# Kernel optimization log

Measured on AMD Instinct MI355X. Metric: run time of the kernel, lower is better.

The kernel has to match this reference:

```python
import jax, jax.numpy as jnp
import numpy as np

B, S, E, H = 2, 2048, 1024, 16
DK = E // H


def setup_inputs() -> dict:
    key = jax.random.key(0)
    ks = jax.random.split(key, 12)
    scale = 1.0 / np.sqrt(E)
    return {
        "query": jax.random.normal(ks[0], (B, S, E), jnp.float32),
        "key": jax.random.normal(ks[1], (B, S, E), jnp.float32),
        "value": jax.random.normal(ks[2], (B, S, E), jnp.float32),
        "key_padding_mask": jnp.ones((B, S, S), jnp.int32),
        "Wq": jax.random.normal(ks[3], (E, E), jnp.float32) * scale,
        "bq": jax.random.normal(ks[4], (E,), jnp.float32) * scale,
        "Wk": jax.random.normal(ks[5], (E, E), jnp.float32) * scale,
        "bk": jax.random.normal(ks[6], (E,), jnp.float32) * scale,
        "Wv": jax.random.normal(ks[7], (E, E), jnp.float32) * scale,
        "bv": jax.random.normal(ks[8], (E,), jnp.float32) * scale,
        "Wo": jax.random.normal(ks[9], (E, E), jnp.float32) * scale,
        "bo": jax.random.normal(ks[10], (E,), jnp.float32) * scale,
    }


def reference(query, key, value, key_padding_mask, Wq, bq, Wk, bk, Wv, bv, Wo, bo):
    b = query.shape[0]
    # torch Linear: x @ W.T + b ; then split heads -> [b, h, t, d_k]
    q = (query @ Wq.T + bq).reshape(b, -1, H, DK).transpose(0, 2, 1, 3)
    k = (key @ Wk.T + bk).reshape(b, -1, H, DK).transpose(0, 2, 1, 3)
    v = (value @ Wv.T + bv).reshape(b, -1, H, DK).transpose(0, 2, 1, 3)
    scores = jnp.einsum("bhqd,bhkd->bhqk", q, k) / np.sqrt(DK)  # [b,h,Tq,Tk]
    mask = (key_padding_mask[:, None, :, :] == 0)  # [b,1,Tq,Tk]
    scores = jnp.where(mask, -jnp.inf, scores)
    attn = jax.nn.softmax(scores, axis=-1)
    attn = jnp.where(mask, 0.0, attn)
    x = jnp.einsum("bhqk,bhkd->bhqd", attn, v)  # [b,h,Tq,d_k]
    x = x.transpose(0, 2, 1, 3).reshape(b, -1, H * DK)  # [b,Tq,E]
    return x @ Wo.T + bo
```

## Files before the change

### kernel.cpp

```cpp
#include <hip/hip_runtime.h>
#include <hip/hip_bf16.h>
#include <cstdint>
#include <cstddef>

#define BB 2
#define SS 2048
#define EE 1024
#define HH 16
#define DKK 64

typedef __bf16 bf16;
typedef __bf16 bf16x8 __attribute__((ext_vector_type(8)));
typedef float f32x4 __attribute__((ext_vector_type(4)));

__device__ __forceinline__ void ldg2lds16(const void* g, void* l) {
  __builtin_amdgcn_global_load_lds(
      (const __attribute__((address_space(1))) unsigned int*)g,
      (__attribute__((address_space(3))) unsigned int*)l, 16, 0, 0);
}

__global__ __launch_bounds__(256) void detect_kernel(
    const unsigned int* __restrict__ q, int* __restrict__ flag) {
  const int t = threadIdx.x;
  int cnt = 0;
#pragma unroll
  for (int i = 0; i < 4; i++) {
    unsigned int v = q[t * 4 + i];
    unsigned int e = (v >> 7) & 0xFF;
    cnt += (e >= 110 && e <= 140) ? 1 : 0;
  }
  __shared__ int s;
  if (t == 0) s = 0;
  __syncthreads();
  atomicAdd(&s, cnt);
  __syncthreads();
  if (t == 0) *flag = (s < 512) ? 1 : 0;
}

struct ConvArgs {
  const void* src[11];
  void* dst[11];
  int n[11];
};

__global__ __launch_bounds__(256) void convert_kernel(
    ConvArgs a, const int* __restrict__ flag) {
  const int j = blockIdx.y;
  const int n = a.n[j];
  const int i0 = (blockIdx.x * 256 + threadIdx.x) * 8;
  if (i0 >= n) return;
  bf16* d = (bf16*)a.dst[j];
  if (*flag) {
    const float* s = (const float*)a.src[j];
    float4 f0 = ((const float4*)(s + i0))[0];
    float4 f1 = ((const float4*)(s + i0))[1];
    union { bf16 h[8]; uint4 u; } t;
    t.h[0] = (bf16)f0.x; t.h[1] = (bf16)f0.y;
    t.h[2] = (bf16)f0.z; t.h[3] = (bf16)f0.w;
    t.h[4] = (bf16)f1.x; t.h[5] = (bf16)f1.y;
    t.h[6] = (bf16)f1.z; t.h[7] = (bf16)f1.w;
    *(uint4*)(d + i0) = t.u;
  } else {
    uint4 v = *(const uint4*)((const bf16*)a.src[j] + i0);
    *(uint4*)(d + i0) = v;
  }
}

__global__ __launch_bounds__(256) void mask_summary_kernel(
    const int* __restrict__ mask, unsigned char* __restrict__ msum) {
  const int bid = blockIdx.x;
  const int kt = bid & 31;
  const int qt = (bid >> 5) & 15;
  const int b = bid >> 9;
  const int t = threadIdx.x;
  const int r = t >> 1;
  const int c0 = (t & 1) * 32;
  const int* p = mask + ((size_t)(b * SS + qt * 128 + r)) * SS + kt * 64 + c0;
  bool all1 = true, any1 = false;
#pragma unroll
  for (int i = 0; i < 8; i++) {
    int4 v = ((const int4*)p)[i];
    all1 = all1 && (v.x != 0) && (v.y != 0) && (v.z != 0) && (v.w != 0);
    any1 = any1 || (v.x != 0) || (v.y != 0) || (v.z != 0) || (v.w != 0);
  }
  __shared__ int sall, sany;
  if (t == 0) { sall = 1; sany = 0; }
  __syncthreads();
  if (!all1) atomicAnd(&sall, 0);
  if (any1) atomicOr(&sany, 1);
  __syncthreads();
  if (t == 0) msum[bid] = sall ? 1 : (sany ? 2 : 0);
}

template <int BM, int BN, int WGM, int WGN, typename OutT>
__device__ __forceinline__ void gemm_bt_core(
    const bf16* __restrict__ A, const bf16* __restrict__ W,
    const bf16* __restrict__ bias, OutT* __restrict__ out, int mode) {
  constexpr int BK = 32;
  constexpr int WM = BM / WGM, WN = BN / WGN;
  constexpr int MI = WM / 16, NI = WN / 16;
  constexpr int Kd = 1024, Nd = 1024;

  __shared__ __align__(16) bf16 As[BM * BK];
  __shared__ __align__(16) bf16 Bs[BN * BK];

  const int tid = threadIdx.x;
  const int wid = tid >> 6, lane = tid & 63;
  const int lr = lane & 15, lg = lane >> 4;
  const int wm = (wid / WGN) * WM, wn = (wid % WGN) * WN;
  const int m0 = blockIdx.y * BM, n0 = blockIdx.x * BN;

  f32x4 acc[MI][NI] = {};

  const int sr = tid >> 2;
  const int scol = (tid & 3) * 8;

  for (int k0 = 0; k0 < Kd; k0 += BK) {
#pragma unroll
    for (int i = 0; i < BM / 64; i++)
      ldg2lds16(A + (size_t)(m0 + sr + i * 64) * Kd + k0 + scol,
                &As[(sr + i * 64) * BK + scol]);
#pragma unroll
    for (int i = 0; i < BN / 64; i++)
      ldg2lds16(W + (size_t)(n0 + sr + i * 64) * Kd + k0 + scol,
                &Bs[(sr + i * 64) * BK + scol]);
    __syncthreads();
    bf16x8 af[MI], bfr[NI];
#pragma unroll
    for (int mi = 0; mi < MI; mi++)
      af[mi] = *(const bf16x8*)&As[(wm + mi * 16 + lr) * BK + lg * 8];
#pragma unroll
    for (int ni = 0; ni < NI; ni++)
      bfr[ni] = *(const bf16x8*)&Bs[(wn + ni * 16 + lr) * BK + lg * 8];
#pragma unroll
    for (int mi = 0; mi < MI; mi++)
#pragma unroll
      for (int ni = 0; ni < NI; ni++)
        acc[mi][ni] = __builtin_amdgcn_mfma_f32_16x16x32_bf16(
            af[mi], bfr[ni], acc[mi][ni], 0, 0, 0);
    __syncthreads();
  }

  const float scale = (mode == 1) ? 0.125f : 1.0f;

#pragma unroll
  for (int ni = 0; ni < NI; ni++) {
    const int n = n0 + wn + ni * 16 + lr;
    const float bv = (float)bias[n];
#pragma unroll
    for (int mi = 0; mi < MI; mi++) {
      const int m = m0 + wm + mi * 16 + lg * 4;
      f32x4 v = acc[mi][ni];
      if (mode == 2) {
        const int h = n >> 6, d = n & 63;
        const int b = m >> 11, s0v = m & 2047;
        union { bf16 hh[4]; uint2 u; } tmp;
#pragma unroll
        for (int r = 0; r < 4; r++) tmp.hh[r] = (bf16)(v[r] + bv);
        const size_t idx = (((size_t)b * HH + h) * DKK + d) * SS + s0v;
        *(uint2*)((bf16*)out + idx) = tmp.u;
      } else {
#pragma unroll
        for (int r = 0; r < 4; r++)
          out[(size_t)(m + r) * Nd + n] = (OutT)((v[r] + bv) * scale);
      }
    }
  }
}

__global__ __launch_bounds__(256) void qkv_proj_kernel(
    const bf16* __restrict__ q, const bf16* __restrict__ k,
    const bf16* __restrict__ v, const bf16* __restrict__ Wq,
    const bf16* __restrict__ Wk, const bf16* __restrict__ Wv,
    const bf16* __restrict__ bias4, bf16* __restrict__ Qo,
    bf16* __restrict__ Ko, bf16* __restrict__ Vto) {
  const int z = blockIdx.z;
  const bf16* A = z == 0 ? q : (z == 1 ? k : v);
  const bf16* W = z == 0 ? Wq : (z == 1 ? Wk : Wv);
  const bf16* bi = bias4 + z * 1024;
  bf16* out = z == 0 ? Qo : (z == 1 ? Ko : Vto);
  gemm_bt_core<128, 128, 2, 2, bf16>(A, W, bi, out, z == 0 ? 1 : (z == 1 ? 0 : 2));
}

__global__ __launch_bounds__(256) void o_proj_kernel(
    const bf16* __restrict__ X, const bf16* __restrict__ Wo,
    const bf16* __restrict__ bo, float* __restrict__ out) {
  gemm_bt_core<64, 128, 1, 4, float>(X, Wo, bo, out, 0);
}

__global__ __launch_bounds__(256, 4) void flash_kernel(
    const bf16* __restrict__ Qb, const bf16* __restrict__ Kb,
    const bf16* __restrict__ Vt, const int* __restrict__ mask,
    const unsigned char* __restrict__ msum, bf16* __restrict__ X) {
  const int flat = blockIdx.x;
  const int bh = flat & 31;
  const int qt2 = flat >> 5;
  const int b = bh >> 4;
  const int h = bh & 15;

  const bf16* Qg = Qb + ((size_t)(b * SS + qt2 * 64)) * EE + h * 64;
  const bf16* Kg = Kb + ((size_t)(b * SS)) * EE + h * 64;
  const bf16* Vg = Vt + ((size_t)(b * HH + h)) * DKK * SS;

  __shared__ __align__(16) bf16 QPs[4608];
  __shared__ __align__(16) bf16 Ks[2 * 64 * 32];
  __shared__ __align__(16) bf16 Vs[2 * 64 * 32];

  const int tid = threadIdx.x;
  const int wid = tid >> 6, lane = tid & 63;
  const int lr = lane & 15, lg = lane >> 4;

#pragma unroll
  for (int j = 0; j < 2; j++) {
    const int u = j * 256 + tid;
    const int kk = u >> 8, row = (u >> 2) & 63, c = (u & 3) * 8;
    ldg2lds16(Qg + (size_t)row * EE + kk * 32 + c, &QPs[u * 8]);
  }
  __syncthreads();

  bf16x8 qf[2];
#pragma unroll
  for (int kk = 0; kk < 2; kk++)
    qf[kk] = *(const bf16x8*)&QPs[kk * 2048 + (wid * 16 + lr) * 32 + lg * 8];
  __syncthreads();

  float mrow[4], lrow[4];
  f32x4 ot[4] = {};
#pragma unroll
  for (int r = 0; r < 4; r++) { mrow[r] = -1e30f; lrow[r] = 0.f; }

  bf16* Pw = &QPs[wid * 1152];

  for (int kt = 0; kt < SS / 64; kt++) {
    const unsigned char sm = msum[(b * 16 + (qt2 >> 1)) * 32 + kt];
    if (sm == 0) continue;

#pragma unroll
    for (int j = 0; j < 2; j++) {
      const int u = j * 256 + tid;
      const int kk = u >> 8, row = (u >> 2) & 63, c = (u & 3) * 8;
      ldg2lds16(Kg + (size_t)(kt * 64 + row) * EE + kk * 32 + c, &Ks[u * 8]);
      ldg2lds16(Vg + (size_t)row * SS + kt * 64 + kk * 32 + c, &Vs[u * 8]);
    }
    __syncthreads();

    f32x4 sc[4] = {};
#pragma unroll
    for (int kk = 0; kk < 2; kk++)
#pragma unroll
      for (int ni = 0; ni < 4; ni++) {
        const bf16x8 kf =
            *(const bf16x8*)&Ks[kk * 2048 + (ni * 16 + lr) * 32 + lg * 8];
        sc[ni] = __builtin_amdgcn_mfma_f32_16x16x32_bf16(qf[kk], kf, sc[ni],
                                                         0, 0, 0);
      }

    if (sm == 2) {
#pragma unroll
      for (int ni = 0; ni < 4; ni++)
#pragma unroll
        for (int r = 0; r < 4; r++) {
          const int qq = qt2 * 64 + wid * 16 + lg * 4 + r;
          const int kk2 = kt * 64 + ni * 16 + lr;
          if (mask[((size_t)b * SS + qq) * SS + kk2] == 0) sc[ni][r] = -1e30f;
        }
    }

    float al[4], mn[4], rs[4];
#pragma unroll
    for (int r = 0; r < 4; r++) {
      float t = fmaxf(fmaxf(sc[0][r], sc[1][r]), fmaxf(sc[2][r], sc[3][r]));
#pragma unroll
      for (int off = 8; off >= 1; off >>= 1) t = fmaxf(t, __shfl_xor(t, off));
      mn[r] = fmaxf(mrow[r], t);
      al[r] = __expf(mrow[r] - mn[r]);
      mrow[r] = mn[r];
      rs[r] = 0.f;
    }
    if (sm == 2) {
#pragma unroll
      for (int ni = 0; ni < 4; ni++)
#pragma unroll
        for (int r = 0; r < 4; r++) {
          const float pv =
              (sc[ni][r] > -5e29f) ? __expf(sc[ni][r] - mn[r]) : 0.f;
          rs[r] += pv;
          Pw[(lg * 4 + r) * 72 + ni * 16 + lr] = (bf16)pv;
        }
    } else {
#pragma unroll
      for (int ni = 0; ni < 4; ni++)
#pragma unroll
        for (int r = 0; r < 4; r++) {
          const float pv = __expf(sc[ni][r] - mn[r]);
          rs[r] += pv;
          Pw[(lg * 4 + r) * 72 + ni * 16 + lr] = (bf16)pv;
        }
    }
#pragma unroll
    for (int r = 0; r < 4; r++) {
#pragma unroll
      for (int off = 8; off >= 1; off >>= 1) rs[r] += __shfl_xor(rs[r], off);
      lrow[r] = lrow[r] * al[r] + rs[r];
    }

#pragma unroll
    for (int di = 0; di < 4; di++)
#pragma unroll
      for (int r = 0; r < 4; r++) ot[di][r] *= al[r];

#pragma unroll
    for (int kk = 0; kk < 2; kk++) {
      const bf16x8 pf = *(const bf16x8*)&Pw[lr * 72 + kk * 32 + lg * 8];
#pragma unroll
      for (int di = 0; di < 4; di++) {
        const bf16x8 vf =
            *(const bf16x8*)&Vs[kk * 2048 + (di * 16 + lr) * 32 + lg * 8];
        ot[di] = __builtin_amdgcn_mfma_f32_16x16x32_bf16(pf, vf, ot[di],
                                                         0, 0, 0);
      }
    }
    __syncthreads();
  }

#pragma unroll
  for (int r = 0; r < 4; r++) {
    const float linv = (lrow[r] > 0.f) ? 1.0f / lrow[r] : 0.f;
    const int q = qt2 * 64 + wid * 16 + lg * 4 + r;
    bf16* xp = X + ((size_t)b * SS + q) * EE + h * 64;
#pragma unroll
    for (int di = 0; di < 4; di++)
      xp[di * 16 + lr] = (bf16)(ot[di][r] * linv);
  }
}

extern "C" void kernel_launch(void* const* d_in, const int* in_sizes, int n_in,
                              void* d_out, int out_size, void* d_ws,
                              size_t ws_size, hipStream_t stream) {
  const int* mask = (const int*)d_in[3];

  const size_t NIN = (size_t)BB * SS * EE;
  const size_t NW = (size_t)EE * EE;

  char* p = (char*)d_ws;
  bf16* cq = (bf16*)p;   p += NIN * 2;
  bf16* ck = (bf16*)p;   p += NIN * 2;
  bf16* cv = (bf16*)p;   p += NIN * 2;
  bf16* cWq = (bf16*)p;  p += NW * 2;
  bf16* cWk = (bf16*)p;  p += NW * 2;
  bf16* cWv = (bf16*)p;  p += NW * 2;
  bf16* cWo = (bf16*)p;  p += NW * 2;
  bf16* cb = (bf16*)p;   p += 4 * 1024 * 2;
  unsigned char* msum = (unsigned char*)p; p += 1024;
  int* flag = (int*)p;   p += 1024;
  bf16* Qb = (bf16*)p;   p += NIN * 2;
  bf16* Kb = (bf16*)p;   p += NIN * 2;
  bf16* Vt = (bf16*)p;   p += NIN * 2;
  bf16* X = (bf16*)p;    p += NIN * 2;

  const size_t need = (size_t)(p - (char*)d_ws);
  if (ws_size < need) return;

  detect_kernel<<<dim3(1), dim3(256), 0, stream>>>(
      (const unsigned int*)d_in[0], flag);

  ConvArgs ca;
  ca.src[0] = d_in[0];   ca.dst[0] = cq;        ca.n[0] = (int)NIN;
  ca.src[1] = d_in[1];   ca.dst[1] = ck;        ca.n[1] = (int)NIN;
  ca.src[2] = d_in[2];   ca.dst[2] = cv;        ca.n[2] = (int)NIN;
  ca.src[3] = d_in[4];   ca.dst[3] = cWq;       ca.n[3] = (int)NW;
  ca.src[4] = d_in[6];   ca.dst[4] = cWk;       ca.n[4] = (int)NW;
  ca.src[5] = d_in[8];   ca.dst[5] = cWv;       ca.n[5] = (int)NW;
  ca.src[6] = d_in[10];  ca.dst[6] = cWo;       ca.n[6] = (int)NW;
  ca.src[7] = d_in[5];   ca.dst[7] = cb;        ca.n[7] = 1024;
  ca.src[8] = d_in[7];   ca.dst[8] = cb + 1024; ca.n[8] = 1024;
  ca.src[9] = d_in[9];   ca.dst[9] = cb + 2048; ca.n[9] = 1024;
  ca.src[10] = d_in[11]; ca.dst[10] = cb + 3072; ca.n[10] = 1024;
  convert_kernel<<<dim3(2048, 11), dim3(256), 0, stream>>>(ca, flag);

  mask_summary_kernel<<<dim3(BB * 16 * 32), dim3(256), 0, stream>>>(mask, msum);

  qkv_proj_kernel<<<dim3(8, 32, 3), dim3(256), 0, stream>>>(
      cq, ck, cv, cWq, cWk, cWv, cb, Qb, Kb, Vt);

  flash_kernel<<<dim3(1024), dim3(256), 0, stream>>>(
      Qb, Kb, Vt, mask, msum, X);

  o_proj_kernel<<<dim3(8, 64), dim3(256), 0, stream>>>(X, cWo, cb + 3072,
                                                       (float*)d_out);
}
```

Measured before the change: 322.4 us.

## Enlarge flash query tile to 128 rows and XOR-swizzle LDS chunks

```diff
diff --git a/kernel.cpp b/kernel.cpp
--- a/kernel.cpp
+++ b/kernel.cpp
@@ -113,25 +113,26 @@
   f32x4 acc[MI][NI] = {};
 
   const int sr = tid >> 2;
-  const int scol = (tid & 3) * 8;
+  const int scol = ((tid & 3) ^ (sr & 3)) * 8;
+  const int rchunk = (lg ^ (lr & 3)) * 8;
 
   for (int k0 = 0; k0 < Kd; k0 += BK) {
 #pragma unroll
     for (int i = 0; i < BM / 64; i++)
       ldg2lds16(A + (size_t)(m0 + sr + i * 64) * Kd + k0 + scol,
-                &As[(sr + i * 64) * BK + scol]);
+                &As[(sr + i * 64) * BK + (tid & 3) * 8]);
 #pragma unroll
     for (int i = 0; i < BN / 64; i++)
       ldg2lds16(W + (size_t)(n0 + sr + i * 64) * Kd + k0 + scol,
-                &Bs[(sr + i * 64) * BK + scol]);
+                &Bs[(sr + i * 64) * BK + (tid & 3) * 8]);
     __syncthreads();
     bf16x8 af[MI], bfr[NI];
 #pragma unroll
     for (int mi = 0; mi < MI; mi++)
-      af[mi] = *(const bf16x8*)&As[(wm + mi * 16 + lr) * BK + lg * 8];
+      af[mi] = *(const bf16x8*)&As[(wm + mi * 16 + lr) * BK + rchunk];
 #pragma unroll
     for (int ni = 0; ni < NI; ni++)
-      bfr[ni] = *(const bf16x8*)&Bs[(wn + ni * 16 + lr) * BK + lg * 8];
+      bfr[ni] = *(const bf16x8*)&Bs[(wn + ni * 16 + lr) * BK + rchunk];
 #pragma unroll
     for (int mi = 0; mi < MI; mi++)
 #pragma unroll
@@ -188,149 +189,178 @@
   gemm_bt_core<64, 128, 1, 4, float>(X, Wo, bo, out, 0);
 }
 
-__global__ __launch_bounds__(256, 4) void flash_kernel(
+__global__ __launch_bounds__(256, 2) void flash_kernel(
     const bf16* __restrict__ Qb, const bf16* __restrict__ Kb,
     const bf16* __restrict__ Vt, const int* __restrict__ mask,
     const unsigned char* __restrict__ msum, bf16* __restrict__ X) {
   const int flat = blockIdx.x;
   const int bh = flat & 31;
-  const int qt2 = flat >> 5;
+  const int qt = flat >> 5;
   const int b = bh >> 4;
   const int h = bh & 15;
 
-  const bf16* Qg = Qb + ((size_t)(b * SS + qt2 * 64)) * EE + h * 64;
+  const bf16* Qg = Qb + ((size_t)(b * SS + qt * 128)) * EE + h * 64;
   const bf16* Kg = Kb + ((size_t)(b * SS)) * EE + h * 64;
   const bf16* Vg = Vt + ((size_t)(b * HH + h)) * DKK * SS;
 
-  __shared__ __align__(16) bf16 QPs[4608];
-  __shared__ __align__(16) bf16 Ks[2 * 64 * 32];
-  __shared__ __align__(16) bf16 Vs[2 * 64 * 32];
+  __shared__ __align__(16) bf16 QPs[8704];
+  __shared__ __align__(16) bf16 Ks[4096];
+  __shared__ __align__(16) bf16 Vs[4096];
 
   const int tid = threadIdx.x;
   const int wid = tid >> 6, lane = tid & 63;
   const int lr = lane & 15, lg = lane >> 4;
-
-#pragma unroll
-  for (int j = 0; j < 2; j++) {
+  const int rchunk = (lg ^ (lr & 3)) * 8;
+
+#pragma unroll
+  for (int j = 0; j < 4; j++) {
     const int u = j * 256 + tid;
-    const int kk = u >> 8, row = (u >> 2) & 63, c = (u & 3) * 8;
-    ldg2lds16(Qg + (size_t)row * EE + kk * 32 + c, &QPs[u * 8]);
-  }
-  __syncthreads();
-
-  bf16x8 qf[2];
-#pragma unroll
-  for (int kk = 0; kk < 2; kk++)
-    qf[kk] = *(const bf16x8*)&QPs[kk * 2048 + (wid * 16 + lr) * 32 + lg * 8];
-  __syncthreads();
-
-  float mrow[4], lrow[4];
-  f32x4 ot[4] = {};
-#pragma unroll
-  for (int r = 0; r < 4; r++) { mrow[r] = -1e30f; lrow[r] = 0.f; }
-
-  bf16* Pw = &QPs[wid * 1152];
+    const int kk = u >> 9, row = (u >> 2) & 127, c = u & 3;
+    ldg2lds16(Qg + (size_t)row * EE + kk * 32 + ((c ^ (row & 3)) * 8),
+              &QPs[u * 8]);
+  }
+  __syncthreads();
+
+  bf16x8 qf[2][2];
+#pragma unroll
+  for (int mi = 0; mi < 2; mi++)
+#pragma unroll
+    for (int kk = 0; kk < 2; kk++)
+      qf[mi][kk] = *(const bf16x8*)
+          &QPs[kk * 4096 + (wid * 32 + mi * 16 + lr) * 32 + rchunk];
+  __syncthreads();
+
+  float mrow[2][4], lrow[2][4];
+  f32x4 ot[2][4] = {};
+#pragma unroll
+  for (int mi = 0; mi < 2; mi++)
+#pragma unroll
+    for (int r = 0; r < 4; r++) { mrow[mi][r] = -1e30f; lrow[mi][r] = 0.f; }
+
+  bf16* Pw = &QPs[wid * 2176];
 
   for (int kt = 0; kt < SS / 64; kt++) {
-    const unsigned char sm = msum[(b * 16 + (qt2 >> 1)) * 32 + kt];
+    const unsigned char sm = msum[(b * 16 + qt) * 32 + kt];
     if (sm == 0) continue;
 
 #pragma unroll
     for (int j = 0; j < 2; j++) {
       const int u = j * 256 + tid;
-      const int kk = u >> 8, row = (u >> 2) & 63, c = (u & 3) * 8;
-      ldg2lds16(Kg + (size_t)(kt * 64 + row) * EE + kk * 32 + c, &Ks[u * 8]);
-      ldg2lds16(Vg + (size_t)row * SS + kt * 64 + kk * 32 + c, &Vs[u * 8]);
+      const int kk = u >> 8, row = (u >> 2) & 63, c = u & 3;
+      const int sc8 = (c ^ (row & 3)) * 8;
+      ldg2lds16(Kg + (size_t)(kt * 64 + row) * EE + kk * 32 + sc8, &Ks[u * 8]);
+      ldg2lds16(Vg + (size_t)row * SS + kt * 64 + kk * 32 + sc8, &Vs[u * 8]);
     }
     __syncthreads();
 
-    f32x4 sc[4] = {};
+    f32x4 sc[2][4] = {};
 #pragma unroll
     for (int kk = 0; kk < 2; kk++)
 #pragma unroll
       for (int ni = 0; ni < 4; ni++) {
         const bf16x8 kf =
-            *(const bf16x8*)&Ks[kk * 2048 + (ni * 16 + lr) * 32 + lg * 8];
-        sc[ni] = __builtin_amdgcn_mfma_f32_16x16x32_bf16(qf[kk], kf, sc[ni],
-                                                         0, 0, 0);
+            *(const bf16x8*)&Ks[kk * 2048 + (ni * 16 + lr) * 32 + rchunk];
+#pragma unroll
+        for (int mi = 0; mi < 2; mi++)
+          sc[mi][ni] = __builtin_amdgcn_mfma_f32_16x16x32_bf16(
+              qf[mi][kk], kf, sc[mi][ni], 0, 0, 0);
       }
 
     if (sm == 2) {
 #pragma unroll
-      for (int ni = 0; ni < 4; ni++)
-#pragma unroll
-        for (int r = 0; r < 4; r++) {
-          const int qq = qt2 * 64 + wid * 16 + lg * 4 + r;
-          const int kk2 = kt * 64 + ni * 16 + lr;
-          if (mask[((size_t)b * SS + qq) * SS + kk2] == 0) sc[ni][r] = -1e30f;
-        }
-    }
-
-    float al[4], mn[4], rs[4];
-#pragma unroll
-    for (int r = 0; r < 4; r++) {
-      float t = fmaxf(fmaxf(sc[0][r], sc[1][r]), fmaxf(sc[2][r], sc[3][r]));
-#pragma unroll
-      for (int off = 8; off >= 1; off >>= 1) t = fmaxf(t, __shfl_xor(t, off));
-      mn[r] = fmaxf(mrow[r], t);
-      al[r] = __expf(mrow[r] - mn[r]);
-      mrow[r] = mn[r];
-      rs[r] = 0.f;
-    }
-    if (sm == 2) {
-#pragma unroll
-      for (int ni = 0; ni < 4; ni++)
-#pragma unroll
-        for (int r = 0; r < 4; r++) {
-          const float pv =
-              (sc[ni][r] > -5e29f) ? __expf(sc[ni][r] - mn[r]) : 0.f;
-          rs[r] += pv;
-          Pw[(lg * 4 + r) * 72 + ni * 16 + lr] = (bf16)pv;
-        }
-    } else {
-#pragma unroll
-      for (int ni = 0; ni < 4; ni++)
-#pragma unroll
-        for (int r = 0; r < 4; r++) {
-          const float pv = __expf(sc[ni][r] - mn[r]);
-          rs[r] += pv;
-          Pw[(lg * 4 + r) * 72 + ni * 16 + lr] = (bf16)pv;
-        }
-    }
-#pragma unroll
-    for (int r = 0; r < 4; r++) {
-#pragma unroll
-      for (int off = 8; off >= 1; off >>= 1) rs[r] += __shfl_xor(rs[r], off);
-      lrow[r] = lrow[r] * al[r] + rs[r];
-    }
-
-#pragma unroll
-    for (int di = 0; di < 4; di++)
-#pragma unroll
-      for (int r = 0; r < 4; r++) ot[di][r] *= al[r];
+      for (int mi = 0; mi < 2; mi++)
+#pragma unroll
+        for (int ni = 0; ni < 4; ni++)
+#pragma unroll
+          for (int r = 0; r < 4; r++) {
+            const int qq = qt * 128 + wid * 32 + mi * 16 + lg * 4 + r;
+            const int kk2 = kt * 64 + ni * 16 + lr;
+            if (mask[((size_t)b * SS + qq) * SS + kk2] == 0)
+              sc[mi][ni][r] = -1e30f;
+          }
+    }
+
+    float al[2][4];
+#pragma unroll
+    for (int mi = 0; mi < 2; mi++) {
+      float mn[4], rs[4];
+#pragma unroll
+      for (int r = 0; r < 4; r++) {
+        float t = fmaxf(fmaxf(sc[mi][0][r], sc[mi][1][r]),
+                        fmaxf(sc[mi][2][r], sc[mi][3][r]));
+#pragma unroll
+        for (int off = 8; off >= 1; off >>= 1) t = fmaxf(t, __shfl_xor(t, off));
+        mn[r] = fmaxf(mrow[mi][r], t);
+        al[mi][r] = __expf(mrow[mi][r] - mn[r]);
+        mrow[mi][r] = mn[r];
+        rs[r] = 0.f;
+      }
+      if (sm == 2) {
+#pragma unroll
+        for (int ni = 0; ni < 4; ni++)
+#pragma unroll
+          for (int r = 0; r < 4; r++) {
+            const float pv =
+                (sc[mi][ni][r] > -5e29f) ? __expf(sc[mi][ni][r] - mn[r]) : 0.f;
+            rs[r] += pv;
+            Pw[(mi * 16 + lg * 4 + r) * 68 + ni * 16 + lr] = (bf16)pv;
+          }
+      } else {
+#pragma unroll
+        for (int ni = 0; ni < 4; ni++)
+#pragma unroll
+          for (int r = 0; r < 4; r++) {
+            const float pv = __expf(sc[mi][ni][r] - mn[r]);
+            rs[r] += pv;
+            Pw[(mi * 16 + lg * 4 + r) * 68 + ni * 16 + lr] = (bf16)pv;
+          }
+      }
+#pragma unroll
+      for (int r = 0; r < 4; r++) {
+#pragma unroll
+        for (int off = 8; off >= 1; off >>= 1) rs[r] += __shfl_xor(rs[r], off);
+        lrow[mi][r] = lrow[mi][r] * al[mi][r] + rs[r];
+      }
+    }
+
+#pragma unroll
+    for (int mi = 0; mi < 2; mi++)
+#pragma unroll
+      for (int di = 0; di < 4; di++)
+#pragma unroll
+        for (int r = 0; r < 4; r++) ot[mi][di][r] *= al[mi][r];
 
 #pragma unroll
     for (int kk = 0; kk < 2; kk++) {
-      const bf16x8 pf = *(const bf16x8*)&Pw[lr * 72 + kk * 32 + lg * 8];
+      bf16x8 pf[2];
+#pragma unroll
+      for (int mi = 0; mi < 2; mi++)
+        pf[mi] = *(const bf16x8*)
+            &Pw[(mi * 16 + lr) * 68 + kk * 32 + lg * 8];
 #pragma unroll
       for (int di = 0; di < 4; di++) {
         const bf16x8 vf =
-            *(const bf16x8*)&Vs[kk * 2048 + (di * 16 + lr) * 32 + lg * 8];
-        ot[di] = __builtin_amdgcn_mfma_f32_16x16x32_bf16(pf, vf, ot[di],
-                                                         0, 0, 0);
+            *(const bf16x8*)&Vs[kk * 2048 + (di * 16 + lr) * 32 + rchunk];
+#pragma unroll
+        for (int mi = 0; mi < 2; mi++)
+          ot[mi][di] = __builtin_amdgcn_mfma_f32_16x16x32_bf16(
+              pf[mi], vf, ot[mi][di], 0, 0, 0);
       }
     }
     __syncthreads();
   }
 
 #pragma unroll
-  for (int r = 0; r < 4; r++) {
-    const float linv = (lrow[r] > 0.f) ? 1.0f / lrow[r] : 0.f;
-    const int q = qt2 * 64 + wid * 16 + lg * 4 + r;
-    bf16* xp = X + ((size_t)b * SS + q) * EE + h * 64;
-#pragma unroll
-    for (int di = 0; di < 4; di++)
-      xp[di * 16 + lr] = (bf16)(ot[di][r] * linv);
+  for (int mi = 0; mi < 2; mi++) {
+#pragma unroll
+    for (int r = 0; r < 4; r++) {
+      const float linv = (lrow[mi][r] > 0.f) ? 1.0f / lrow[mi][r] : 0.f;
+      const int q = qt * 128 + wid * 32 + mi * 16 + lg * 4 + r;
+      bf16* xp = X + ((size_t)b * SS + q) * EE + h * 64;
+#pragma unroll
+      for (int di = 0; di < 4; di++)
+        xp[di * 16 + lr] = (bf16)(ot[mi][di][r] * linv);
+    }
   }
 }
 
@@ -383,7 +413,7 @@
   qkv_proj_kernel<<<dim3(8, 32, 3), dim3(256), 0, stream>>>(
       cq, ck, cv, cWq, cWk, cWv, cb, Qb, Kb, Vt);
 
-  flash_kernel<<<dim3(1024), dim3(256), 0, stream>>>(
+  flash_kernel<<<dim3(512), dim3(256), 0, stream>>>(
       Qb, Kb, Vt, mask, msum, X);
 
   o_proj_kernel<<<dim3(8, 64), dim3(256), 0, stream>>>(X, cWo, cb + 3072,
```

Result: slower. 339.3 us (+5.3%).
